# Optimization experiments

Measured on AMD Instinct MI355X. Metric: run time of the kernel, lower is better.

The kernel has to match this reference:

```python
import jax, jax.numpy as jnp
import numpy as np

B, S, E, H = 4, 2048, 512, 1024

def setup_inputs() -> dict:
    key = jax.random.key(0)
    ks = jax.random.split(key, 8)
    s = 1.0 / np.sqrt(H)
    return {
        "hidden_states": jax.random.normal(ks[0], (B, S, H), jnp.float32),
        "external_embeddings": jax.random.normal(ks[1], (B, E, H), jnp.float32),
        "Wq": jax.random.normal(ks[2], (H, H), jnp.float32) * s,
        "bq": jax.random.normal(ks[3], (H,), jnp.float32) * 0.02,
        "Wk": jax.random.normal(ks[4], (H, H), jnp.float32) * s,
        "bk": jax.random.normal(ks[5], (H,), jnp.float32) * 0.02,
        "Wv": jax.random.normal(ks[6], (H, H), jnp.float32) * s,
        "bv": jax.random.normal(ks[7], (H,), jnp.float32) * 0.02,
    }

def reference(hidden_states, external_embeddings, Wq, bq, Wk, bk, Wv, bv):
    # Projections (torch Linear semantics: here weights stored as [in,out])
    q = hidden_states @ Wq + bq              # [B,S,H]
    k_tok = hidden_states @ Wk + bk          # [B,S,H]
    v_tok = hidden_states @ Wv + bv          # [B,S,H]
    k_ext = external_embeddings @ Wk + bk    # [B,E,H]
    v_ext = external_embeddings @ Wv + bv    # [B,E,H]
    # Each token attends to [its own key] ++ [external keys]; NO 1/sqrt(d) scaling
    # and NO head splitting, matching the original forward exactly.
    s_self = jnp.einsum('bsh,bsh->bs', q, k_tok)[..., None]   # [B,S,1]
    s_ext = jnp.einsum('bsh,beh->bse', q, k_ext)              # [B,S,E]
    scores = jnp.concatenate([s_self, s_ext], axis=-1)        # [B,S,1+E]
    probs = jax.nn.softmax(scores, axis=-1)
    ctx = probs[..., :1] * v_tok + jnp.einsum('bse,beh->bsh', probs[..., 1:], v_ext)
    return ctx  # [B,S,H]
```

## Files before the change

kernel.cpp:

```cpp
#include <hip/hip_runtime.h>
#include <stdint.h>

#define BB 4
#define SS 2048
#define EE 512
#define HH 1024

typedef _Float16 f16;
typedef __attribute__((ext_vector_type(8))) _Float16 f16x8;
typedef __attribute__((ext_vector_type(4))) _Float16 f16x4;
typedef __attribute__((ext_vector_type(4))) float f32x4;

__device__ __forceinline__ void async16(void* lds, const void* g) {
  __builtin_amdgcn_global_load_lds(
      (const __attribute__((address_space(1))) unsigned int*)g,
      (__attribute__((address_space(3))) unsigned int*)lds, 16, 0, 0);
}

#define MFMA16 __builtin_amdgcn_mfma_f32_16x16x32_f16

__global__ __launch_bounds__(256) void cast_kernel(const float* __restrict__ xh32,
                                                   const float* __restrict__ xe32,
                                                   f16* __restrict__ xh,
                                                   f16* __restrict__ xe) {
  const int i = blockIdx.x * 256 + threadIdx.x;
  const int n4h = 8192 * HH / 4;
  const float* src = i < n4h ? xh32 : xe32;
  f16* dst = i < n4h ? xh : xe;
  const int k = i < n4h ? i : i - n4h;
  const float4 v = ((const float4*)src)[k];
  f16x4 o;
  o.x = (f16)v.x; o.y = (f16)v.y; o.z = (f16)v.z; o.w = (f16)v.w;
  ((f16x4*)dst)[k] = o;
}

__global__ void wsplit_kernel(const float* __restrict__ Wq, const float* __restrict__ Wk,
                              const float* __restrict__ Wv, f16* __restrict__ wt_hi,
                              f16* __restrict__ wt_lo) {
  __shared__ float tile[32][33];
  const int k0 = blockIdx.x * 32;
  const int n0g = blockIdx.y * 32;
  const int which = n0g >> 10;
  const float* W = which == 0 ? Wq : (which == 1 ? Wk : Wv);
  const int n0 = n0g & 1023;
  const int tx = threadIdx.x, ty = threadIdx.y;
#pragma unroll
  for (int i = 0; i < 32; i += 8)
    tile[ty + i][tx] = W[(size_t)(k0 + ty + i) * 1024 + n0 + tx];
  __syncthreads();
#pragma unroll
  for (int i = 0; i < 32; i += 8) {
    const int np = n0g + ty + i;
    const float v = tile[tx][ty + i];
    const size_t idx = (size_t)np * 1024 + k0 + tx;
    const f16 h = (f16)v;
    wt_hi[idx] = h;
    wt_lo[idx] = (f16)(v - (float)h);
  }
}

__global__ __launch_bounds__(512, 2) void proj_kernel(
    const f16* __restrict__ xh, const f16* __restrict__ xe,
    const f16* __restrict__ wt_hi, const f16* __restrict__ wt_lo,
    const float* __restrict__ bq, const float* __restrict__ bk,
    const float* __restrict__ bv, f16* __restrict__ q_hi, f16* __restrict__ q_lo,
    f16* __restrict__ kt, f16* __restrict__ vt,
    f16* __restrict__ ke_hi, f16* __restrict__ ke_lo, f16* __restrict__ veT) {
  const int g = blockIdx.x;
  const int j = g & 7;
  const int s = g >> 3;
  int mrow0, colB0;
  bool ext = false, splitB = false;
  if (s < 20) {
    splitB = true;
    if (s < 16) {
      colB0 = (s >> 2) * 256;
      mrow0 = ((s & 3) * 8 + j) * 256;
    } else {
      ext = true;
      colB0 = 1024 + (s - 16) * 256;
      mrow0 = j * 256;
    }
  } else {
    const int s2 = s - 20;
    if (s2 < 32) {
      colB0 = (4 + (s2 >> 2)) * 256;
      mrow0 = ((s2 & 3) * 8 + j) * 256;
    } else {
      ext = true;
      colB0 = 1024 + (4 + (s2 - 32)) * 256;
      mrow0 = j * 256;
    }
  }
  const int NT = splitB ? 32 : 16;

  __shared__ f16 lds[65536];

  const int tid = threadIdx.x;
  const int wave = tid >> 6, lane = tid & 63;
  const int wm = wave >> 2, wn = wave & 3;
  const int frow = lane & 15, qd = lane >> 4;

  const f16* A0 = (ext ? xe : xh) + (size_t)mrow0 * HH;
  const f16* Bhi = wt_hi + (size_t)colB0 * HH;
  const f16* Blo = wt_lo + (size_t)colB0 * HH;

  const int srow = tid >> 2;
  const int scol = ((tid & 3) ^ ((srow >> 1) & 3)) * 8;
  const size_t gO0 = (size_t)srow * HH + scol;
  const size_t gO1 = (size_t)(128 + srow) * HH + scol;
  const int ldst0 = (wave * 64) * 8;
  const int ldst1 = (512 + wave * 64) * 8;

  int offA[8], offB[4];
#pragma unroll
  for (int i = 0; i < 8; ++i) {
    const int r = wm * 128 + i * 16 + frow;
    offA[i] = r * 32 + ((qd ^ ((r >> 1) & 3)) * 8);
  }
#pragma unroll
  for (int jj = 0; jj < 4; ++jj) {
    const int r = wn * 64 + jj * 16 + frow;
    offB[jj] = r * 32 + ((qd ^ ((r >> 1) & 3)) * 8);
  }

  f32x4 acc[8][4];
#pragma unroll
  for (int i = 0; i < 8; ++i)
#pragma unroll
    for (int jj = 0; jj < 4; ++jj)
#pragma unroll
      for (int r = 0; r < 4; ++r) acc[i][jj][r] = 0.0f;

  {
    f16* dA0 = &lds[0];
    f16* dB0 = &lds[32768];
    f16* dA1 = &lds[8192];
    f16* dB1 = &lds[32768 + 8192];
    async16(&dA0[ldst0], A0 + gO0);       async16(&dA0[ldst1], A0 + gO1);
    async16(&dB0[ldst0], Bhi + gO0);      async16(&dB0[ldst1], Bhi + gO1);
    async16(&dA1[ldst0], A0 + 32 + gO0);  async16(&dA1[ldst1], A0 + 32 + gO1);
    async16(&dB1[ldst0], Bhi + 32 + gO0); async16(&dB1[ldst1], Bhi + 32 + gO1);
  }
  asm volatile("s_waitcnt vmcnt(4)" ::: "memory");
  __builtin_amdgcn_s_barrier();

  for (int t = 0; t < NT; ++t) {
    const int cur = t & 1, nxt = cur ^ 1;
    const bool st = (t + 1 < NT);
    const int kn = ((t + 1) & 15) * 64;
    const f16* An = A0 + kn;
    const f16* Bn = (((t + 1) & 16) ? Blo : Bhi) + kn;
    const f16* lA0 = &lds[(cur * 2 + 0) * 8192];
    const f16* lB0 = &lds[32768 + (cur * 2 + 0) * 8192];
    const f16* lA1 = &lds[(cur * 2 + 1) * 8192];
    const f16* lB1 = &lds[32768 + (cur * 2 + 1) * 8192];
    f16* sA0 = &lds[(nxt * 2 + 0) * 8192];
    f16* sB0 = &lds[32768 + (nxt * 2 + 0) * 8192];
    f16* sA1 = &lds[(nxt * 2 + 1) * 8192];
    f16* sB1 = &lds[32768 + (nxt * 2 + 1) * 8192];

    f16x8 a[8], b0, b1;

#pragma unroll
    for (int i = 0; i < 8; ++i) a[i] = *(const f16x8*)&lA0[offA[i]];
    b0 = *(const f16x8*)&lB0[offB[0]];
    b1 = *(const f16x8*)&lB0[offB[1]];
    if (st) { async16(&sA0[ldst0], An + gO0); async16(&sA0[ldst1], An + gO1); }
    __builtin_amdgcn_s_barrier();
    __builtin_amdgcn_s_setprio(1);
#pragma unroll
    for (int i = 0; i < 8; ++i) {
      acc[i][0] = MFMA16(a[i], b0, acc[i][0], 0, 0, 0);
      acc[i][1] = MFMA16(a[i], b1, acc[i][1], 0, 0, 0);
    }
    __builtin_amdgcn_s_setprio(0);
    __builtin_amdgcn_s_barrier();

    b0 = *(const f16x8*)&lB0[offB[2]];
    b1 = *(const f16x8*)&lB0[offB[3]];
    if (st) { async16(&sB0[ldst0], Bn + gO0); async16(&sB0[ldst1], Bn + gO1); }
    __builtin_amdgcn_s_barrier();
    __builtin_amdgcn_s_setprio(1);
#pragma unroll
    for (int i = 0; i < 8; ++i) {
      acc[i][2] = MFMA16(a[i], b0, acc[i][2], 0, 0, 0);
      acc[i][3] = MFMA16(a[i], b1, acc[i][3], 0, 0, 0);
    }
    __builtin_amdgcn_s_setprio(0);
    if (t == NT - 1) {
      asm volatile("s_waitcnt vmcnt(0)" ::: "memory");
    } else {
      asm volatile("s_waitcnt vmcnt(4)" ::: "memory");
    }
    __builtin_amdgcn_s_barrier();

#pragma unroll
    for (int i = 0; i < 8; ++i) a[i] = *(const f16x8*)&lA1[offA[i]];
    b0 = *(const f16x8*)&lB1[offB[0]];
    b1 = *(const f16x8*)&lB1[offB[1]];
    if (st) { async16(&sA1[ldst0], An + 32 + gO0); async16(&sA1[ldst1], An + 32 + gO1); }
    __builtin_amdgcn_s_barrier();
    __builtin_amdgcn_s_setprio(1);
#pragma unroll
    for (int i = 0; i < 8; ++i) {
      acc[i][0] = MFMA16(a[i], b0, acc[i][0], 0, 0, 0);
      acc[i][1] = MFMA16(a[i], b1, acc[i][1], 0, 0, 0);
    }
    __builtin_amdgcn_s_setprio(0);
    __builtin_amdgcn_s_barrier();

    b0 = *(const f16x8*)&lB1[offB[2]];
    b1 = *(const f16x8*)&lB1[offB[3]];
    if (st) { async16(&sB1[ldst0], Bn + 32 + gO0); async16(&sB1[ldst1], Bn + 32 + gO1); }
    __builtin_amdgcn_s_barrier();
    __builtin_amdgcn_s_setprio(1);
#pragma unroll
    for (int i = 0; i < 8; ++i) {
      acc[i][2] = MFMA16(a[i], b0, acc[i][2], 0, 0, 0);
      acc[i][3] = MFMA16(a[i], b1, acc[i][3], 0, 0, 0);
    }
    __builtin_amdgcn_s_setprio(0);
    asm volatile("s_waitcnt vmcnt(4)" ::: "memory");
    __builtin_amdgcn_s_barrier();
  }

  const int er0 = wm * 128 + qd * 4;
  const int ec0 = wn * 64 + frow;
  float bias[4];
#pragma unroll
  for (int jj = 0; jj < 4; ++jj) {
    const int c = colB0 + ec0 + jj * 16;
    bias[jj] = c < 1024 ? bq[c] : (c < 2048 ? bk[c - 1024] : bv[c - 2048]);
  }

  if (!ext) {
    if (colB0 < 1024) {
#pragma unroll
      for (int jj = 0; jj < 4; ++jj) {
        const int c = colB0 + ec0 + jj * 16;
#pragma unroll
        for (int i = 0; i < 8; ++i)
#pragma unroll
          for (int r = 0; r < 4; ++r) {
            const int row = mrow0 + er0 + i * 16 + r;
            const float val = acc[i][jj][r] + bias[jj];
            const size_t idx = (size_t)row * HH + c;
            const f16 h = (f16)val;
            q_hi[idx] = h;
            q_lo[idx] = (f16)(val - (float)h);
          }
      }
    } else if (colB0 < 2048) {
#pragma unroll
      for (int jj = 0; jj < 4; ++jj) {
        const int c = colB0 + ec0 + jj * 16 - 1024;
#pragma unroll
        for (int i = 0; i < 8; ++i)
#pragma unroll
          for (int r = 0; r < 4; ++r) {
            const int row = mrow0 + er0 + i * 16 + r;
            kt[(size_t)row * HH + c] = (f16)(acc[i][jj][r] + bias[jj]);
          }
      }
    } else {
#pragma unroll
      for (int jj = 0; jj < 4; ++jj) {
        const int c = colB0 + ec0 + jj * 16 - 2048;
#pragma unroll
        for (int i = 0; i < 8; ++i)
#pragma unroll
          for (int r = 0; r < 4; ++r) {
            const int row = mrow0 + er0 + i * 16 + r;
            vt[(size_t)row * HH + c] = (f16)(acc[i][jj][r] + bias[jj]);
          }
      }
    }
  } else {
    if (colB0 < 2048) {
#pragma unroll
      for (int jj = 0; jj < 4; ++jj) {
        const int c = colB0 + ec0 + jj * 16 - 1024;
#pragma unroll
        for (int i = 0; i < 8; ++i)
#pragma unroll
          for (int r = 0; r < 4; ++r) {
            const int row = mrow0 + er0 + i * 16 + r;
            const float val = acc[i][jj][r] + bias[jj];
            const size_t idx = (size_t)row * HH + c;
            const f16 h = (f16)val;
            ke_hi[idx] = h;
            ke_lo[idx] = (f16)(val - (float)h);
          }
      }
    } else {
      f16* tl = lds;
      const int b = mrow0 >> 9, e0 = mrow0 & 511;
      const int h0 = colB0 - 2048;
#pragma unroll
      for (int p = 0; p < 2; ++p) {
        __syncthreads();
        if ((wn >> 1) == p) {
          const int hL = (wn & 1) * 64 + frow;
#pragma unroll
          for (int jj = 0; jj < 4; ++jj)
#pragma unroll
            for (int i = 0; i < 8; ++i)
#pragma unroll
              for (int r = 0; r < 4; ++r) {
                const int e = er0 + i * 16 + r;
                tl[(hL + jj * 16) * 264 + e] = (f16)(acc[i][jj][r] + bias[jj]);
              }
        }
        __syncthreads();
        for (int c = tid; c < 128 * 32; c += 512) {
          const int hL = c >> 5, ch = c & 31;
          const f16x8 v = *(const f16x8*)&tl[hL * 264 + ch * 8];
          *(f16x8*)&veT[(size_t)(b * HH + h0 + p * 128 + hL) * EE + e0 + ch * 8] = v;
        }
      }
    }
  }
}

__global__ __launch_bounds__(512, 2) void score_kernel(
    const f16* __restrict__ q_hi, const f16* __restrict__ q_lo,
    const f16* __restrict__ ke_hi, const f16* __restrict__ ke_lo,
    float* __restrict__ s_part) {
  const int b = blockIdx.z & 3;
  const int khalf = blockIdx.z >> 2;
  const int mtile = blockIdx.y;
  const int ntile = blockIdx.x;

  __shared__ f16 lds[49152];

  const int tid = threadIdx.x;
  const int wave = tid >> 6, lane = tid & 63;
  const int wm = wave >> 1, wn = wave & 1;
  const int frow = lane & 15, qd = lane >> 4;

  const size_t aoff = ((size_t)b * SS + mtile * 256) * HH + khalf * 512;
  const size_t boff = ((size_t)b * EE + ntile * 128) * HH + khalf * 512;
  const f16* Ah = q_hi + aoff;
  const f16* Al = q_lo + aoff;
  const f16* Bh = ke_hi + boff;
  const f16* Bl = ke_lo + boff;

  const int srow = tid >> 2;
  const int scol = ((tid & 3) ^ ((srow >> 1) & 3)) * 8;
  const size_t gA0 = (size_t)srow * HH + scol;
  const size_t gA1 = (size_t)(128 + srow) * HH + scol;
  const int ldstA0 = (wave * 64) * 8;
  const int ldstA1 = (512 + wave * 64) * 8;
  const int ldstB0 = (wave * 64) * 8;

  int offA[4], offB[4];
#pragma unroll
  for (int i = 0; i < 4; ++i) {
    const int r = wm * 64 + i * 16 + frow;
    offA[i] = r * 32 + ((qd ^ ((r >> 1) & 3)) * 8);
  }
#pragma unroll
  for (int jj = 0; jj < 4; ++jj) {
    const int r = wn * 64 + jj * 16 + frow;
    offB[jj] = r * 32 + ((qd ^ ((r >> 1) & 3)) * 8);
  }

  f32x4 acc[4][4];
#pragma unroll
  for (int i = 0; i < 4; ++i)
#pragma unroll
    for (int jj = 0; jj < 4; ++jj)
#pragma unroll
      for (int r = 0; r < 4; ++r) acc[i][jj][r] = 0.0f;

  {
    f16* dAh = &lds[0];
    f16* dAl = &lds[8192];
    f16* dBh = &lds[16384];
    f16* dBl = &lds[20480];
    async16(&dAh[ldstA0], Ah + gA0); async16(&dAh[ldstA1], Ah + gA1);
    async16(&dBh[ldstB0], Bh + gA0);
    async16(&dBl[ldstB0], Bl + gA0);
    async16(&dAl[ldstA0], Al + gA0); async16(&dAl[ldstA1], Al + gA1);
  }
  asm volatile("s_waitcnt vmcnt(3)" ::: "memory");
  __builtin_amdgcn_s_barrier();

  for (int t = 0; t < 16; ++t) {
    const int cur = t & 1, nxt = cur ^ 1;
    const bool st = (t < 15);
    const int kk = (t + 1) * 32;
    const f16* lAh = &lds[cur * 24576];
    const f16* lAl = &lds[cur * 24576 + 8192];
    const f16* lBh = &lds[cur * 24576 + 16384];
    const f16* lBl = &lds[cur * 24576 + 20480];
    f16* sAh = &lds[nxt * 24576];
    f16* sAl = &lds[nxt * 24576 + 8192];
    f16* sBh = &lds[nxt * 24576 + 16384];
    f16* sBl = &lds[nxt * 24576 + 20480];

    f16x8 ah[4], bh[4], x[4];

#pragma unroll
    for (int i = 0; i < 4; ++i) ah[i] = *(const f16x8*)&lAh[offA[i]];
#pragma unroll
    for (int jj = 0; jj < 4; ++jj) bh[jj] = *(const f16x8*)&lBh[offB[jj]];
    if (st) {
      async16(&sAh[ldstA0], Ah + kk + gA0); async16(&sAh[ldstA1], Ah + kk + gA1);
      async16(&sBh[ldstB0], Bh + kk + gA0);
    }
    __builtin_amdgcn_s_barrier();
    __builtin_amdgcn_s_setprio(1);
#pragma unroll
    for (int i = 0; i < 4; ++i)
#pragma unroll
      for (int jj = 0; jj < 4; ++jj)
        acc[i][jj] = MFMA16(ah[i], bh[jj], acc[i][jj], 0, 0, 0);
    __builtin_amdgcn_s_setprio(0);
    if (st) { asm volatile("s_waitcnt vmcnt(5)" ::: "memory"); }
    else    { asm volatile("s_waitcnt vmcnt(2)" ::: "memory"); }
    __builtin_amdgcn_s_barrier();

#pragma unroll
    for (int jj = 0; jj < 4; ++jj) x[jj] = *(const f16x8*)&lBl[offB[jj]];
    if (st) async16(&sBl[ldstB0], Bl + kk + gA0);
    __builtin_amdgcn_s_barrier();
    __builtin_amdgcn_s_setprio(1);
#pragma unroll
    for (int i = 0; i < 4; ++i)
#pragma unroll
      for (int jj = 0; jj < 4; ++jj)
        acc[i][jj] = MFMA16(ah[i], x[jj], acc[i][jj], 0, 0, 0);
    __builtin_amdgcn_s_setprio(0);
    if (st) { asm volatile("s_waitcnt vmcnt(4)" ::: "memory"); }
    else    { asm volatile("s_waitcnt vmcnt(0)" ::: "memory"); }
    __builtin_amdgcn_s_barrier();

#pragma unroll
    for (int i = 0; i < 4; ++i) x[i] = *(const f16x8*)&lAl[offA[i]];
    if (st) { async16(&sAl[ldstA0], Al + kk + gA0); async16(&sAl[ldstA1], Al + kk + gA1); }
    __builtin_amdgcn_s_barrier();
    __builtin_amdgcn_s_setprio(1);
#pragma unroll
    for (int i = 0; i < 4; ++i)
#pragma unroll
      for (int jj = 0; jj < 4; ++jj)
        acc[i][jj] = MFMA16(x[i], bh[jj], acc[i][jj], 0, 0, 0);
    __builtin_amdgcn_s_setprio(0);
    if (st) { asm volatile("s_waitcnt vmcnt(3)" ::: "memory"); }
    __builtin_amdgcn_s_barrier();
  }

  float* dst = s_part + (size_t)khalf * BB * SS * EE + (size_t)b * SS * EE;
#pragma unroll
  for (int jj = 0; jj < 4; ++jj) {
    const int e = ntile * 128 + wn * 64 + jj * 16 + frow;
#pragma unroll
    for (int i = 0; i < 4; ++i)
#pragma unroll
      for (int r = 0; r < 4; ++r) {
        const int s = mtile * 256 + wm * 64 + i * 16 + qd * 4 + r;
        dst[(size_t)s * EE + e] = acc[i][jj][r];
      }
  }
}

__global__ __launch_bounds__(256) void softmax_kernel(
    const f16* __restrict__ q_hi, const f16* __restrict__ q_lo,
    const f16* __restrict__ kt, const float* __restrict__ s_part,
    f16* __restrict__ probs, float* __restrict__ p_self) {
  const int t = blockIdx.x * 4 + (threadIdx.x >> 6);
  const int lane = threadIdx.x & 63;

  const size_t base = (size_t)t * HH;
  float ss = 0.f;
#pragma unroll
  for (int it = 0; it < 4; ++it) {
    const int off = it * 256 + lane * 4;
    const f16x4 qh = *(const f16x4*)&q_hi[base + off];
    const f16x4 ql = *(const f16x4*)&q_lo[base + off];
    const f16x4 kh = *(const f16x4*)&kt[base + off];
    ss += ((float)qh.x + (float)ql.x) * (float)kh.x;
    ss += ((float)qh.y + (float)ql.y) * (float)kh.y;
    ss += ((float)qh.z + (float)ql.z) * (float)kh.z;
    ss += ((float)qh.w + (float)ql.w) * (float)kh.w;
  }
#pragma unroll
  for (int m = 32; m > 0; m >>= 1) ss += __shfl_xor(ss, m, 64);

  const float* r0 = s_part + (size_t)t * EE;
  const float* r1 = s_part + (size_t)BB * SS * EE + (size_t)t * EE;
  const float4 a0 = *(const float4*)&r0[lane * 4];
  const float4 a1 = *(const float4*)&r0[256 + lane * 4];
  const float4 c0 = *(const float4*)&r1[lane * 4];
  const float4 c1 = *(const float4*)&r1[256 + lane * 4];
  const float v0x = a0.x + c0.x, v0y = a0.y + c0.y, v0z = a0.z + c0.z, v0w = a0.w + c0.w;
  const float v1x = a1.x + c1.x, v1y = a1.y + c1.y, v1z = a1.z + c1.z, v1w = a1.w + c1.w;
  float m = fmaxf(fmaxf(fmaxf(v0x, v0y), fmaxf(v0z, v0w)),
                  fmaxf(fmaxf(v1x, v1y), fmaxf(v1z, v1w)));
#pragma unroll
  for (int sh = 32; sh > 0; sh >>= 1) m = fmaxf(m, __shfl_xor(m, sh, 64));
  m = fmaxf(m, ss);
  const float e0 = __expf(v0x - m), e1 = __expf(v0y - m);
  const float e2 = __expf(v0z - m), e3 = __expf(v0w - m);
  const float e4 = __expf(v1x - m), e5 = __expf(v1y - m);
  const float e6 = __expf(v1z - m), e7 = __expf(v1w - m);
  float sum = ((e0 + e1) + (e2 + e3)) + ((e4 + e5) + (e6 + e7));
#pragma unroll
  for (int sh = 32; sh > 0; sh >>= 1) sum += __shfl_xor(sum, sh, 64);
  const float es = __expf(ss - m);
  const float inv = 1.0f / (sum + es);
  f16x4 p0, p1;
  p0.x = (f16)(e0 * inv); p0.y = (f16)(e1 * inv);
  p0.z = (f16)(e2 * inv); p0.w = (f16)(e3 * inv);
  p1.x = (f16)(e4 * inv); p1.y = (f16)(e5 * inv);
  p1.z = (f16)(e6 * inv); p1.w = (f16)(e7 * inv);
  *(f16x4*)&probs[(size_t)t * EE + lane * 4] = p0;
  *(f16x4*)&probs[(size_t)t * EE + 256 + lane * 4] = p1;
  if (lane == 0) p_self[t] = es * inv;
}

__global__ __launch_bounds__(512, 2) void pv_kernel(
    const f16* __restrict__ probs, const f16* __restrict__ veT,
    const float* __restrict__ p_self, const f16* __restrict__ vt,
    float* __restrict__ out) {
  const int b = blockIdx.z;
  const int mtile = blockIdx.y;
  const int ntile = blockIdx.x;

  __shared__ f16 lds[36864];

  const int tid = threadIdx.x;
  const int wave = tid >> 6, lane = tid & 63;
  const int wm = wave >> 1, wn = wave & 1;
  const int frow = lane & 15, qd = lane >> 4;

  const size_t aoff = ((size_t)b * SS + mtile * 256) * EE;
  const size_t boff = ((size_t)b * HH + ntile * 128) * EE;
  const f16* A = probs + aoff;
  const f16* Bv = veT + boff;

  const int srow = tid >> 2;
  const int scol = ((tid & 3) ^ ((srow >> 1) & 3)) * 8;
  const size_t gA0 = (size_t)srow * EE + scol;
  const size_t gA1 = (size_t)(128 + srow) * EE + scol;
  const int ldstA0 = (wave * 64) * 8;
  const int ldstA1 = (512 + wave * 64) * 8;
  const int ldstB0 = (wave * 64) * 8;

  int offA[4], offB[4];
#pragma unroll
  for (int i = 0; i < 4; ++i) {
    const int r = wm * 64 + i * 16 + frow;
    offA[i] = r * 32 + ((qd ^ ((r >> 1) & 3)) * 8);
  }
#pragma unroll
  for (int jj = 0; jj < 4; ++jj) {
    const int r = wn * 64 + jj * 16 + frow;
    offB[jj] = r * 32 + ((qd ^ ((r >> 1) & 3)) * 8);
  }

  f32x4 acc[4][4];
#pragma unroll
  for (int i = 0; i < 4; ++i)
#pragma unroll
    for (int jj = 0; jj < 4; ++jj)
#pragma unroll
      for (int r = 0; r < 4; ++r) acc[i][jj][r] = 0.0f;

  {
    f16* dA0 = &lds[0], *dB0 = &lds[8192];
    f16* dA1 = &lds[12288], *dB1 = &lds[12288 + 8192];
    async16(&dA0[ldstA0], A + gA0); async16(&dA0[ldstA1], A + gA1);
    async16(&dB0[ldstB0], Bv + gA0);
    async16(&dA1[ldstA0], A + 32 + gA0); async16(&dA1[ldstA1], A + 32 + gA1);
    async16(&dB1[ldstB0], Bv + 32 + gA0);
  }
  asm volatile("s_waitcnt vmcnt(3)" ::: "memory");
  __builtin_amdgcn_s_barrier();

  int cur = 0, stg = 2;
  for (int t = 0; t < 16; ++t) {
    const bool st = (t < 14);
    const int kk = (t + 2) * 32;
    const f16* lA = &lds[cur * 12288];
    const f16* lB = &lds[cur * 12288 + 8192];
    f16* sA = &lds[stg * 12288];
    f16* sB = &lds[stg * 12288 + 8192];

    f16x8 a[4], b[4];

#pragma unroll
    for (int i = 0; i < 4; ++i) a[i] = *(const f16x8*)&lA[offA[i]];
    b[0] = *(const f16x8*)&lB[offB[0]];
    b[1] = *(const f16x8*)&lB[offB[1]];
    if (st) { async16(&sA[ldstA0], A + kk + gA0); async16(&sA[ldstA1], A + kk + gA1); }
    __builtin_amdgcn_s_barrier();
    __builtin_amdgcn_s_setprio(1);
#pragma unroll
    for (int i = 0; i < 4; ++i) {
      acc[i][0] = MFMA16(a[i], b[0], acc[i][0], 0, 0, 0);
      acc[i][1] = MFMA16(a[i], b[1], acc[i][1], 0, 0, 0);
    }
    __builtin_amdgcn_s_setprio(0);
    __builtin_amdgcn_s_barrier();

    b[2] = *(const f16x8*)&lB[offB[2]];
    b[3] = *(const f16x8*)&lB[offB[3]];
    if (st) async16(&sB[ldstB0], Bv + kk + gA0);
    __builtin_amdgcn_s_barrier();
    __builtin_amdgcn_s_setprio(1);
#pragma unroll
    for (int i = 0; i < 4; ++i) {
      acc[i][2] = MFMA16(a[i], b[2], acc[i][2], 0, 0, 0);
      acc[i][3] = MFMA16(a[i], b[3], acc[i][3], 0, 0, 0);
    }
    __builtin_amdgcn_s_setprio(0);
    if (t < 14)      { asm volatile("s_waitcnt vmcnt(3)" ::: "memory"); }
    else if (t == 14){ asm volatile("s_waitcnt vmcnt(0)" ::: "memory"); }
    __builtin_amdgcn_s_barrier();

    cur = (cur == 2) ? 0 : cur + 1;
    stg = (stg == 2) ? 0 : stg + 1;
  }

#pragma unroll
  for (int jj = 0; jj < 4; ++jj) {
    const int h = ntile * 128 + wn * 64 + jj * 16 + frow;
#pragma unroll
    for (int i = 0; i < 4; ++i)
#pragma unroll
      for (int r = 0; r < 4; ++r) {
        const int s = mtile * 256 + wm * 64 + i * 16 + qd * 4 + r;
        const size_t t = (size_t)b * SS + s;
        __builtin_nontemporal_store(
            acc[i][jj][r] + p_self[t] * (float)vt[t * HH + h], &out[t * HH + h]);
      }
  }
}

extern "C" void kernel_launch(void* const* d_in, const int* in_sizes, int n_in,
                              void* d_out, int out_size, void* d_ws, size_t ws_size,
                              hipStream_t stream) {
  const float* hidden = (const float*)d_in[0];
  const float* ext    = (const float*)d_in[1];
  const float* Wq = (const float*)d_in[2];
  const float* bq = (const float*)d_in[3];
  const float* Wk = (const float*)d_in[4];
  const float* bk = (const float*)d_in[5];
  const float* Wv = (const float*)d_in[6];
  const float* bv = (const float*)d_in[7];
  float* out = (float*)d_out;

  char* ws = (char*)d_ws;
  size_t off = 0;
  auto alloc = [&](size_t bytes) {
    char* p = ws + off;
    off += (bytes + 255) & ~(size_t)255;
    return p;
  };
  const size_t TOK = 8192, EXT = 2048;
  f16* xh    = (f16*)alloc(TOK * HH * 2);
  f16* xe    = (f16*)alloc(EXT * HH * 2);
  f16* wt_hi = (f16*)alloc(3072ull * HH * 2);
  f16* wt_lo = (f16*)alloc(3072ull * HH * 2);
  f16* q_hi  = (f16*)alloc(TOK * HH * 2);
  f16* q_lo  = (f16*)alloc(TOK * HH * 2);
  f16* kt    = (f16*)alloc(TOK * HH * 2);
  f16* vt    = (f16*)alloc(TOK * HH * 2);
  f16* ke_hi = (f16*)alloc(EXT * HH * 2);
  f16* ke_lo = (f16*)alloc(EXT * HH * 2);
  f16* veT   = (f16*)alloc((size_t)BB * HH * EE * 2);
  float* p_self = (float*)alloc(TOK * 4);
  float* s_part = (float*)alloc(2ull * BB * SS * EE * 4);
  f16* probs    = (f16*)alloc((size_t)BB * SS * EE * 2);

  cast_kernel<<<10240, 256, 0, stream>>>(hidden, ext, xh, xe);
  wsplit_kernel<<<dim3(32, 96), dim3(32, 8), 0, stream>>>(Wq, Wk, Wv, wt_hi, wt_lo);

  proj_kernel<<<448, 512, 0, stream>>>(
      xh, xe, wt_hi, wt_lo, bq, bk, bv,
      q_hi, q_lo, kt, vt, ke_hi, ke_lo, veT);

  score_kernel<<<dim3(4, 8, 8), 512, 0, stream>>>(q_hi, q_lo, ke_hi, ke_lo, s_part);
  softmax_kernel<<<2048, 256, 0, stream>>>(q_hi, q_lo, kt, s_part, probs, p_self);
  pv_kernel<<<dim3(8, 8, 4), 512, 0, stream>>>(probs, veT, p_self, vt, out);
}
```

Measured before the change: 281.1 us.

## Shrink projection tiles to 256x128 with triple-buffered K=32 pipeline and interleaved scheduling

The projection GEMM tile goes from 256x256 to 256x128 columns, so each workgroup holds half the accumulators and about 72KB of LDS. This lets 4 workgroups fit per CU instead of 2, and the grid doubles to 896 blocks. The K loop now steps 32 at a time through a 3-stage LDS ring buffer, and long split (hi+lo) tiles are interleaved with short tiles in groups of 14 to balance load. In exchange, arithmetic intensity per tile drops and the A operand traffic doubles.

```diff
diff --git a/kernel.cpp b/kernel.cpp
--- a/kernel.cpp
+++ b/kernel.cpp
@@ -59,7 +59,7 @@
   }
 }
 
-__global__ __launch_bounds__(512, 2) void proj_kernel(
+__global__ __launch_bounds__(512, 4) void proj_kernel(
     const f16* __restrict__ xh, const f16* __restrict__ xe,
     const f16* __restrict__ wt_hi, const f16* __restrict__ wt_lo,
     const float* __restrict__ bq, const float* __restrict__ bk,
@@ -67,38 +67,45 @@
     f16* __restrict__ kt, f16* __restrict__ vt,
     f16* __restrict__ ke_hi, f16* __restrict__ ke_lo, f16* __restrict__ veT) {
   const int g = blockIdx.x;
-  const int j = g & 7;
-  const int s = g >> 3;
-  int mrow0, colB0;
-  bool ext = false, splitB = false;
-  if (s < 20) {
-    splitB = true;
-    if (s < 16) {
-      colB0 = (s >> 2) * 256;
-      mrow0 = ((s & 3) * 8 + j) * 256;
+  const int grp = g / 14, slot = g % 14;
+  int mrow0, colB0, NT;
+  bool ext = false, split = false;
+  if (slot < 5) {
+    const int li = grp * 5 + slot;
+    split = true;
+    NT = 64;
+    if (li < 256) {
+      colB0 = (li >> 5) * 128;
+      mrow0 = (li & 31) * 256;
     } else {
+      const int l2 = li - 256;
       ext = true;
-      colB0 = 1024 + (s - 16) * 256;
-      mrow0 = j * 256;
+      colB0 = 1024 + (l2 >> 3) * 128;
+      mrow0 = (l2 & 7) * 256;
     }
   } else {
-    const int s2 = s - 20;
-    if (s2 < 32) {
-      colB0 = (4 + (s2 >> 2)) * 256;
-      mrow0 = ((s2 & 3) * 8 + j) * 256;
+    const int si = grp * 9 + (slot - 5);
+    NT = 32;
+    if (si < 256) {
+      colB0 = 1024 + (si >> 5) * 128;
+      mrow0 = (si & 31) * 256;
+    } else if (si < 512) {
+      const int s2 = si - 256;
+      colB0 = 2048 + (s2 >> 5) * 128;
+      mrow0 = (s2 & 31) * 256;
     } else {
+      const int s3 = si - 512;
       ext = true;
-      colB0 = 1024 + (4 + (s2 - 32)) * 256;
-      mrow0 = j * 256;
-    }
-  }
-  const int NT = splitB ? 32 : 16;
-
-  __shared__ f16 lds[65536];
+      colB0 = 2048 + (s3 >> 3) * 128;
+      mrow0 = (s3 & 7) * 256;
+    }
+  }
+
+  __shared__ f16 lds[36864];
 
   const int tid = threadIdx.x;
   const int wave = tid >> 6, lane = tid & 63;
-  const int wm = wave >> 2, wn = wave & 3;
+  const int wm = wave >> 1, wn = wave & 1;
   const int frow = lane & 15, qd = lane >> 4;
 
   const f16* A0 = (ext ? xe : xh) + (size_t)mrow0 * HH;
@@ -107,15 +114,16 @@
 
   const int srow = tid >> 2;
   const int scol = ((tid & 3) ^ ((srow >> 1) & 3)) * 8;
-  const size_t gO0 = (size_t)srow * HH + scol;
-  const size_t gO1 = (size_t)(128 + srow) * HH + scol;
-  const int ldst0 = (wave * 64) * 8;
-  const int ldst1 = (512 + wave * 64) * 8;
-
-  int offA[8], offB[4];
-#pragma unroll
-  for (int i = 0; i < 8; ++i) {
-    const int r = wm * 128 + i * 16 + frow;
+  const size_t gA0 = (size_t)srow * HH + scol;
+  const size_t gA1 = (size_t)(128 + srow) * HH + scol;
+  const int ldstA0 = (wave * 64) * 8;
+  const int ldstA1 = (512 + wave * 64) * 8;
+  const int ldstB0 = (wave * 64) * 8;
+
+  int offA[4], offB[4];
+#pragma unroll
+  for (int i = 0; i < 4; ++i) {
+    const int r = wm * 64 + i * 16 + frow;
     offA[i] = r * 32 + ((qd ^ ((r >> 1) & 3)) * 8);
   }
 #pragma unroll
@@ -124,108 +132,74 @@
     offB[jj] = r * 32 + ((qd ^ ((r >> 1) & 3)) * 8);
   }
 
-  f32x4 acc[8][4];
-#pragma unroll
-  for (int i = 0; i < 8; ++i)
+  f32x4 acc[4][4];
+#pragma unroll
+  for (int i = 0; i < 4; ++i)
 #pragma unroll
     for (int jj = 0; jj < 4; ++jj)
 #pragma unroll
       for (int r = 0; r < 4; ++r) acc[i][jj][r] = 0.0f;
 
   {
-    f16* dA0 = &lds[0];
-    f16* dB0 = &lds[32768];
-    f16* dA1 = &lds[8192];
-    f16* dB1 = &lds[32768 + 8192];
-    async16(&dA0[ldst0], A0 + gO0);       async16(&dA0[ldst1], A0 + gO1);
-    async16(&dB0[ldst0], Bhi + gO0);      async16(&dB0[ldst1], Bhi + gO1);
-    async16(&dA1[ldst0], A0 + 32 + gO0);  async16(&dA1[ldst1], A0 + 32 + gO1);
-    async16(&dB1[ldst0], Bhi + 32 + gO0); async16(&dB1[ldst1], Bhi + 32 + gO1);
-  }
-  asm volatile("s_waitcnt vmcnt(4)" ::: "memory");
+    f16* dA0 = &lds[0], *dB0 = &lds[8192];
+    f16* dA1 = &lds[12288], *dB1 = &lds[12288 + 8192];
+    async16(&dA0[ldstA0], A0 + gA0); async16(&dA0[ldstA1], A0 + gA1);
+    async16(&dB0[ldstB0], Bhi + gA0);
+    async16(&dA1[ldstA0], A0 + 32 + gA0); async16(&dA1[ldstA1], A0 + 32 + gA1);
+    async16(&dB1[ldstB0], Bhi + 32 + gA0);
+  }
+  asm volatile("s_waitcnt vmcnt(3)" ::: "memory");
   __builtin_amdgcn_s_barrier();
 
+  int cur = 0, stg = 2;
   for (int t = 0; t < NT; ++t) {
-    const int cur = t & 1, nxt = cur ^ 1;
-    const bool st = (t + 1 < NT);
-    const int kn = ((t + 1) & 15) * 64;
-    const f16* An = A0 + kn;
-    const f16* Bn = (((t + 1) & 16) ? Blo : Bhi) + kn;
-    const f16* lA0 = &lds[(cur * 2 + 0) * 8192];
-    const f16* lB0 = &lds[32768 + (cur * 2 + 0) * 8192];
-    const f16* lA1 = &lds[(cur * 2 + 1) * 8192];
-    const f16* lB1 = &lds[32768 + (cur * 2 + 1) * 8192];
-    f16* sA0 = &lds[(nxt * 2 + 0) * 8192];
-    f16* sB0 = &lds[32768 + (nxt * 2 + 0) * 8192];
-    f16* sA1 = &lds[(nxt * 2 + 1) * 8192];
-    f16* sB1 = &lds[32768 + (nxt * 2 + 1) * 8192];
-
-    f16x8 a[8], b0, b1;
-
-#pragma unroll
-    for (int i = 0; i < 8; ++i) a[i] = *(const f16x8*)&lA0[offA[i]];
-    b0 = *(const f16x8*)&lB0[offB[0]];
-    b1 = *(const f16x8*)&lB0[offB[1]];
-    if (st) { async16(&sA0[ldst0], An + gO0); async16(&sA0[ldst1], An + gO1); }
+    const bool st = (t < NT - 2);
+    const int kk = t + 2;
+    const int ko = (kk & 31) * 32;
+    const f16* As = A0 + ko;
+    const f16* Bs = ((split && kk >= 32) ? Blo : Bhi) + ko;
+    const f16* lA = &lds[cur * 12288];
+    const f16* lB = &lds[cur * 12288 + 8192];
+    f16* sA = &lds[stg * 12288];
+    f16* sB = &lds[stg * 12288 + 8192];
+
+    f16x8 a[4], b[4];
+
+#pragma unroll
+    for (int i = 0; i < 4; ++i) a[i] = *(const f16x8*)&lA[offA[i]];
+    b[0] = *(const f16x8*)&lB[offB[0]];
+    b[1] = *(const f16x8*)&lB[offB[1]];
+    if (st) { async16(&sA[ldstA0], As + gA0); async16(&sA[ldstA1], As + gA1); }
     __builtin_amdgcn_s_barrier();
     __builtin_amdgcn_s_setprio(1);
 #pragma unroll
-    for (int i = 0; i < 8; ++i) {
-      acc[i][0] = MFMA16(a[i], b0, acc[i][0], 0, 0, 0);
-      acc[i][1] = MFMA16(a[i], b1, acc[i][1], 0, 0, 0);
+    for (int i = 0; i < 4; ++i) {
+      acc[i][0] = MFMA16(a[i], b[0], acc[i][0], 0, 0, 0);
+      acc[i][1] = MFMA16(a[i], b[1], acc[i][1], 0, 0, 0);
     }
     __builtin_amdgcn_s_setprio(0);
     __builtin_amdgcn_s_barrier();
 
-    b0 = *(const f16x8*)&lB0[offB[2]];
-    b1 = *(const f16x8*)&lB0[offB[3]];
-    if (st) { async16(&sB0[ldst0], Bn + gO0); async16(&sB0[ldst1], Bn + gO1); }
+    b[2] = *(const f16x8*)&lB[offB[2]];
+    b[3] = *(const f16x8*)&lB[offB[3]];
+    if (st) async16(&sB[ldstB0], Bs + gA0);
     __builtin_amdgcn_s_barrier();
     __builtin_amdgcn_s_setprio(1);
 #pragma unroll
-    for (int i = 0; i < 8; ++i) {
-      acc[i][2] = MFMA16(a[i], b0, acc[i][2], 0, 0, 0);
-      acc[i][3] = MFMA16(a[i], b1, acc[i][3], 0, 0, 0);
+    for (int i = 0; i < 4; ++i) {
+      acc[i][2] = MFMA16(a[i], b[2], acc[i][2], 0, 0, 0);
+      acc[i][3] = MFMA16(a[i], b[3], acc[i][3], 0, 0, 0);
     }
     __builtin_amdgcn_s_setprio(0);
-    if (t == NT - 1) {
-      asm volatile("s_waitcnt vmcnt(0)" ::: "memory");
-    } else {
-      asm volatile("s_waitcnt vmcnt(4)" ::: "memory");
-    }
-    __builtin_amdgcn_s_barrier();
-
-#pragma unroll
-    for (int i = 0; i < 8; ++i) a[i] = *(const f16x8*)&lA1[offA[i]];
-    b0 = *(const f16x8*)&lB1[offB[0]];
-    b1 = *(const f16x8*)&lB1[offB[1]];
-    if (st) { async16(&sA1[ldst0], An + 32 + gO0); async16(&sA1[ldst1], An + 32 + gO1); }
-    __builtin_amdgcn_s_barrier();
-    __builtin_amdgcn_s_setprio(1);
-#pragma unroll
-    for (int i = 0; i < 8; ++i) {
-      acc[i][0] = MFMA16(a[i], b0, acc[i][0], 0, 0, 0);
-      acc[i][1] = MFMA16(a[i], b1, acc[i][1], 0, 0, 0);
-    }
-    __builtin_amdgcn_s_setprio(0);
-    __builtin_amdgcn_s_barrier();
-
-    b0 = *(const f16x8*)&lB1[offB[2]];
-    b1 = *(const f16x8*)&lB1[offB[3]];
-    if (st) { async16(&sB1[ldst0], Bn + 32 + gO0); async16(&sB1[ldst1], Bn + 32 + gO1); }
-    __builtin_amdgcn_s_barrier();
-    __builtin_amdgcn_s_setprio(1);
-#pragma unroll
-    for (int i = 0; i < 8; ++i) {
-      acc[i][2] = MFMA16(a[i], b0, acc[i][2], 0, 0, 0);
-      acc[i][3] = MFMA16(a[i], b1, acc[i][3], 0, 0, 0);
-    }
-    __builtin_amdgcn_s_setprio(0);
-    asm volatile("s_waitcnt vmcnt(4)" ::: "memory");
-    __builtin_amdgcn_s_barrier();
-  }
-
-  const int er0 = wm * 128 + qd * 4;
+    if (t < NT - 2)       { asm volatile("s_waitcnt vmcnt(3)" ::: "memory"); }
+    else if (t == NT - 2) { asm volatile("s_waitcnt vmcnt(0)" ::: "memory"); }
+    __builtin_amdgcn_s_barrier();
+
+    cur = (cur == 2) ? 0 : cur + 1;
+    stg = (stg == 2) ? 0 : stg + 1;
+  }
+
+  const int er0 = wm * 64 + qd * 4;
   const int ec0 = wn * 64 + frow;
   float bias[4];
 #pragma unroll
@@ -240,7 +214,7 @@
       for (int jj = 0; jj < 4; ++jj) {
         const int c = colB0 + ec0 + jj * 16;
 #pragma unroll
-        for (int i = 0; i < 8; ++i)
+        for (int i = 0; i < 4; ++i)
 #pragma unroll
           for (int r = 0; r < 4; ++r) {
             const int row = mrow0 + er0 + i * 16 + r;
@@ -256,7 +230,7 @@
       for (int jj = 0; jj < 4; ++jj) {
         const int c = colB0 + ec0 + jj * 16 - 1024;
 #pragma unroll
-        for (int i = 0; i < 8; ++i)
+        for (int i = 0; i < 4; ++i)
 #pragma unroll
           for (int r = 0; r < 4; ++r) {
             const int row = mrow0 + er0 + i * 16 + r;
@@ -268,7 +242,7 @@
       for (int jj = 0; jj < 4; ++jj) {
         const int c = colB0 + ec0 + jj * 16 - 2048;
 #pragma unroll
-        for (int i = 0; i < 8; ++i)
+        for (int i = 0; i < 4; ++i)
 #pragma unroll
           for (int r = 0; r < 4; ++r) {
             const int row = mrow0 + er0 + i * 16 + r;
@@ -282,7 +256,7 @@
       for (int jj = 0; jj < 4; ++jj) {
         const int c = colB0 + ec0 + jj * 16 - 1024;
 #pragma unroll
-        for (int i = 0; i < 8; ++i)
+        for (int i = 0; i < 4; ++i)
 #pragma unroll
           for (int r = 0; r < 4; ++r) {
             const int row = mrow0 + er0 + i * 16 + r;
@@ -297,27 +271,23 @@
       f16* tl = lds;
       const int b = mrow0 >> 9, e0 = mrow0 & 511;
       const int h0 = colB0 - 2048;
-#pragma unroll
-      for (int p = 0; p < 2; ++p) {
-        __syncthreads();
-        if ((wn >> 1) == p) {
-          const int hL = (wn & 1) * 64 + frow;
-#pragma unroll
-          for (int jj = 0; jj < 4; ++jj)
-#pragma unroll
-            for (int i = 0; i < 8; ++i)
-#pragma unroll
-              for (int r = 0; r < 4; ++r) {
-                const int e = er0 + i * 16 + r;
-                tl[(hL + jj * 16) * 264 + e] = (f16)(acc[i][jj][r] + bias[jj]);
-              }
-        }
-        __syncthreads();
-        for (int c = tid; c < 128 * 32; c += 512) {
-          const int hL = c >> 5, ch = c & 31;
-          const f16x8 v = *(const f16x8*)&tl[hL * 264 + ch * 8];
-          *(f16x8*)&veT[(size_t)(b * HH + h0 + p * 128 + hL) * EE + e0 + ch * 8] = v;
-        }
+      __syncthreads();
+#pragma unroll
+      for (int jj = 0; jj < 4; ++jj) {
+        const int hL = ec0 + jj * 16;
+#pragma unroll
+        for (int i = 0; i < 4; ++i)
+#pragma unroll
+          for (int r = 0; r < 4; ++r) {
+            const int e = er0 + i * 16 + r;
+            tl[hL * 264 + e] = (f16)(acc[i][jj][r] + bias[jj]);
+          }
+      }
+      __syncthreads();
+      for (int c = tid; c < 128 * 32; c += 512) {
+        const int hL = c >> 5, ch = c & 31;
+        const f16x8 v = *(const f16x8*)&tl[hL * 264 + ch * 8];
+        *(f16x8*)&veT[(size_t)(b * HH + h0 + hL) * EE + e0 + ch * 8] = v;
       }
     }
   }
@@ -679,7 +649,7 @@
   cast_kernel<<<10240, 256, 0, stream>>>(hidden, ext, xh, xe);
   wsplit_kernel<<<dim3(32, 96), dim3(32, 8), 0, stream>>>(Wq, Wk, Wv, wt_hi, wt_lo);
 
-  proj_kernel<<<448, 512, 0, stream>>>(
+  proj_kernel<<<896, 512, 0, stream>>>(
       xh, xe, wt_hi, wt_lo, bq, bk, bv,
       q_hi, q_lo, kt, vt, ke_hi, ke_lo, veT);
 
```

Result: slower. 314.2 us (+11.8%).

## Triple-buffer score GEMM LDS pipeline with two-stage prefetch depth

Applied to the files above, without the earlier changes.

Converts the score kernel's double-buffered LDS pipeline into a three-stage ring, prefetching two k-steps ahead. Mid-iteration vmcnt waits are removed, leaving a single wait per iteration, and the Bh load moves next to the Bl load. This grows LDS to 144KB per block and drops launch bounds to one block per CU. Deeper latency hiding is traded against lower occupancy.

```diff
diff --git a/kernel.cpp b/kernel.cpp
--- a/kernel.cpp
+++ b/kernel.cpp
@@ -323,7 +323,7 @@
   }
 }
 
-__global__ __launch_bounds__(512, 2) void score_kernel(
+__global__ __launch_bounds__(512, 1) void score_kernel(
     const f16* __restrict__ q_hi, const f16* __restrict__ q_lo,
     const f16* __restrict__ ke_hi, const f16* __restrict__ ke_lo,
     float* __restrict__ s_part) {
@@ -332,7 +332,7 @@
   const int mtile = blockIdx.y;
   const int ntile = blockIdx.x;
 
-  __shared__ f16 lds[49152];
+  __shared__ f16 lds[73728];
 
   const int tid = threadIdx.x;
   const int wave = tid >> 6, lane = tid & 63;
@@ -374,31 +374,33 @@
 #pragma unroll
       for (int r = 0; r < 4; ++r) acc[i][jj][r] = 0.0f;
 
-  {
-    f16* dAh = &lds[0];
-    f16* dAl = &lds[8192];
-    f16* dBh = &lds[16384];
-    f16* dBl = &lds[20480];
-    async16(&dAh[ldstA0], Ah + gA0); async16(&dAh[ldstA1], Ah + gA1);
-    async16(&dBh[ldstB0], Bh + gA0);
-    async16(&dBl[ldstB0], Bl + gA0);
-    async16(&dAl[ldstA0], Al + gA0); async16(&dAl[ldstA1], Al + gA1);
-  }
-  asm volatile("s_waitcnt vmcnt(3)" ::: "memory");
+#pragma unroll
+  for (int p = 0; p < 2; ++p) {
+    f16* dAh = &lds[p * 24576];
+    f16* dAl = &lds[p * 24576 + 8192];
+    f16* dBh = &lds[p * 24576 + 16384];
+    f16* dBl = &lds[p * 24576 + 20480];
+    const int ko = p * 32;
+    async16(&dAh[ldstA0], Ah + ko + gA0); async16(&dAh[ldstA1], Ah + ko + gA1);
+    async16(&dBh[ldstB0], Bh + ko + gA0);
+    async16(&dBl[ldstB0], Bl + ko + gA0);
+    async16(&dAl[ldstA0], Al + ko + gA0); async16(&dAl[ldstA1], Al + ko + gA1);
+  }
+  asm volatile("s_waitcnt vmcnt(6)" ::: "memory");
   __builtin_amdgcn_s_barrier();
 
+  int cur = 0, stg = 2;
   for (int t = 0; t < 16; ++t) {
-    const int cur = t & 1, nxt = cur ^ 1;
-    const bool st = (t < 15);
-    const int kk = (t + 1) * 32;
+    const bool st = (t < 14);
+    const int kk = (t + 2) * 32;
     const f16* lAh = &lds[cur * 24576];
     const f16* lAl = &lds[cur * 24576 + 8192];
     const f16* lBh = &lds[cur * 24576 + 16384];
     const f16* lBl = &lds[cur * 24576 + 20480];
-    f16* sAh = &lds[nxt * 24576];
-    f16* sAl = &lds[nxt * 24576 + 8192];
-    f16* sBh = &lds[nxt * 24576 + 16384];
-    f16* sBl = &lds[nxt * 24576 + 20480];
+    f16* sAh = &lds[stg * 24576];
+    f16* sAl = &lds[stg * 24576 + 8192];
+    f16* sBh = &lds[stg * 24576 + 16384];
+    f16* sBl = &lds[stg * 24576 + 20480];
 
     f16x8 ah[4], bh[4], x[4];
 
@@ -408,7 +410,6 @@
     for (int jj = 0; jj < 4; ++jj) bh[jj] = *(const f16x8*)&lBh[offB[jj]];
     if (st) {
       async16(&sAh[ldstA0], Ah + kk + gA0); async16(&sAh[ldstA1], Ah + kk + gA1);
-      async16(&sBh[ldstB0], Bh + kk + gA0);
     }
     __builtin_amdgcn_s_barrier();
     __builtin_amdgcn_s_setprio(1);
@@ -418,13 +419,14 @@
       for (int jj = 0; jj < 4; ++jj)
         acc[i][jj] = MFMA16(ah[i], bh[jj], acc[i][jj], 0, 0, 0);
     __builtin_amdgcn_s_setprio(0);
-    if (st) { asm volatile("s_waitcnt vmcnt(5)" ::: "memory"); }
-    else    { asm volatile("s_waitcnt vmcnt(2)" ::: "memory"); }
     __builtin_amdgcn_s_barrier();
 
 #pragma unroll
     for (int jj = 0; jj < 4; ++jj) x[jj] = *(const f16x8*)&lBl[offB[jj]];
-    if (st) async16(&sBl[ldstB0], Bl + kk + gA0);
+    if (st) {
+      async16(&sBh[ldstB0], Bh + kk + gA0);
+      async16(&sBl[ldstB0], Bl + kk + gA0);
+    }
     __builtin_amdgcn_s_barrier();
     __builtin_amdgcn_s_setprio(1);
 #pragma unroll
@@ -433,13 +435,13 @@
       for (int jj = 0; jj < 4; ++jj)
         acc[i][jj] = MFMA16(ah[i], x[jj], acc[i][jj], 0, 0, 0);
     __builtin_amdgcn_s_setprio(0);
-    if (st) { asm volatile("s_waitcnt vmcnt(4)" ::: "memory"); }
-    else    { asm volatile("s_waitcnt vmcnt(0)" ::: "memory"); }
     __builtin_amdgcn_s_barrier();
 
 #pragma unroll
     for (int i = 0; i < 4; ++i) x[i] = *(const f16x8*)&lAl[offA[i]];
-    if (st) { async16(&sAl[ldstA0], Al + kk + gA0); async16(&sAl[ldstA1], Al + kk + gA1); }
+    if (st) {
+      async16(&sAl[ldstA0], Al + kk + gA0); async16(&sAl[ldstA1], Al + kk + gA1);
+    }
     __builtin_amdgcn_s_barrier();
     __builtin_amdgcn_s_setprio(1);
 #pragma unroll
@@ -448,8 +450,12 @@
       for (int jj = 0; jj < 4; ++jj)
         acc[i][jj] = MFMA16(x[i], bh[jj], acc[i][jj], 0, 0, 0);
     __builtin_amdgcn_s_setprio(0);
-    if (st) { asm volatile("s_waitcnt vmcnt(3)" ::: "memory"); }
-    __builtin_amdgcn_s_barrier();
+    if (t < 14)       { asm volatile("s_waitcnt vmcnt(6)" ::: "memory"); }
+    else if (t == 14) { asm volatile("s_waitcnt vmcnt(0)" ::: "memory"); }
+    __builtin_amdgcn_s_barrier();
+
+    cur = (cur == 2) ? 0 : cur + 1;
+    stg = (stg == 2) ? 0 : stg + 1;
   }
 
   float* dst = s_part + (size_t)khalf * BB * SS * EE + (size_t)b * SS * EE;
```

Result: no change. 282.8 us (+0.6%).
